# Kernel optimization log

Hardware: AMD Instinct MI355X
Metric: run time of the kernel (lower is better)

## Reference

```python
import jax, jax.numpy as jnp
import numpy as np


def _base_grid(B, H, W):
    xs = jnp.arange(W, dtype=jnp.float32)
    ys = jnp.arange(H, dtype=jnp.float32)
    gx, gy = jnp.meshgrid(xs, ys)  # [H,W] each, x varies along W
    return jnp.broadcast_to(jnp.stack([gx, gy], -1)[None], (B, H, W, 2))


def flow_to_grid(flow, accel=None):
    B, _, H, W = flow.shape
    v = 0.5 * flow
    if accel is not None:
        v = v + 0.25 * accel
    vgrid = _base_grid(B, H, W) + jnp.transpose(v, (0, 2, 3, 1))
    gx = 2.0 * vgrid[..., 0] / max(W - 1, 1) - 1.0
    gy = 2.0 * vgrid[..., 1] / max(H - 1, 1) - 1.0
    return jnp.stack([gx, gy], -1)  # [B,H,W,2]


def grid_sample_border(img, grid):
    # img [B,C,H,W], grid [B,Hg,Wg,2] normalized; bilinear, border pad, align_corners=True
    B, C, H, W = img.shape
    Hg, Wg = grid.shape[1], grid.shape[2]
    x = jnp.clip((grid[..., 0] + 1.0) * 0.5 * (W - 1), 0.0, W - 1)
    y = jnp.clip((grid[..., 1] + 1.0) * 0.5 * (H - 1), 0.0, H - 1)
    x0 = jnp.floor(x); y0 = jnp.floor(y)
    x1 = jnp.minimum(x0 + 1.0, W - 1); y1 = jnp.minimum(y0 + 1.0, H - 1)
    wx = (x - x0)[:, None]; wy = (y - y0)[:, None]  # [B,1,Hg,Wg]
    x0i, x1i, y0i, y1i = (a.astype(jnp.int32) for a in (x0, x1, y0, y1))
    flat = img.reshape(B, C, H * W)

    def gat(yi, xi):
        idx = jnp.broadcast_to((yi * W + xi).reshape(B, 1, Hg * Wg), (B, C, Hg * Wg))
        return jnp.take_along_axis(flat, idx, axis=2).reshape(B, C, Hg, Wg)

    v00, v01, v10, v11 = gat(y0i, x0i), gat(y0i, x1i), gat(y1i, x0i), gat(y1i, x1i)
    return v00 * (1 - wx) * (1 - wy) + v01 * wx * (1 - wy) + v10 * (1 - wx) * wy + v11 * wx * wy


def backward_warp(img, flow, accel=None):
    grid = flow_to_grid(flow, accel)
    warped = grid_sample_border(img, grid)
    valid = (jnp.abs(grid[..., 0]) <= 1.0) & (jnp.abs(grid[..., 1]) <= 1.0)
    return warped * valid[:, None].astype(img.dtype)


def local_kernel_warp(img, flow, kernel_params):
    B, C, H, W = img.shape
    k_row = jax.nn.softmax(kernel_params[:, :5], axis=1)   # [B,5,H,W]
    k_col = jax.nn.softmax(kernel_params[:, 5:10], axis=1)
    aniso = jax.nn.sigmoid(kernel_params[:, 10]) + 0.5     # [B,H,W]
    grid = flow_to_grid(flow)                               # [B,H,W,2]
    offsets = jnp.linspace(-2.0, 2.0, 5)
    a3 = aniso[..., None]                                   # [B,H,W,1]
    off_col = offsets.reshape(1, 1, 1, 5) * a3              # [B,H,W,5]
    off_row = offsets.reshape(1, 1, 1, 5) / a3
    zeros = jnp.zeros_like(off_row)
    grid_row = grid[:, :, :, None, :] + jnp.stack([off_row, zeros], -1) * (2.0 / W)
    samples_row = grid_sample_border(img, grid_row.reshape(B, H, W * 5, 2)).reshape(B, C, H, W, 5)
    img_row = jnp.einsum('bchwk,bkhw->bchw', samples_row, k_row)
    grid_base = flow_to_grid(jnp.zeros_like(flow))
    grid_col = grid_base[:, :, :, None, :] + jnp.stack([zeros, off_col], -1) * (2.0 / H)
    samples_col = grid_sample_border(img_row, grid_col.reshape(B, H, W * 5, 2)).reshape(B, C, H, W, 5)
    return jnp.einsum('bchwk,bkhw->bchw', samples_col, k_col)


def conv3x3(x, w, b):
    y = jax.lax.conv_general_dilated(x, w, (1, 1), 'SAME',
                                     dimension_numbers=('NCHW', 'OIHW', 'NCHW'))
    return y + b[None, :, None, None]


def reference(img, features, flow, kernel_params, w1, b1, w2, b2):
    B, _, H, W = img.shape
    Hf, Wf = features.shape[2], features.shape[3]
    warped_img = local_kernel_warp(img, flow, kernel_params)
    flow_scaled = jax.image.resize(flow, (B, 2, Hf, Wf), 'linear') * (Hf / H)
    warped_feat = backward_warp(features, flow_scaled)
    warped_img_down = jax.image.resize(warped_img, (B, 3, Hf, Wf), 'linear')
    x = jnp.concatenate([warped_feat, warped_img_down], axis=1)
    fused = conv3x3(jax.nn.relu(conv3x3(x, w1, b1)), w2, b2)
    return (warped_feat + fused, warped_img)


def setup_inputs() -> dict:
    key = jax.random.key(0)
    ks = jax.random.split(key, 6)
    B, H, W, Hf, Wf, Cf = 4, 512, 512, 256, 256, 96
    return {
        'img': jax.random.uniform(ks[0], (B, 3, H, W), jnp.float32),
        'features': jax.random.normal(ks[1], (B, Cf, Hf, Wf), jnp.float32),
        'flow': jax.random.normal(ks[2], (B, 2, H, W), jnp.float32) * 4.0,
        'kernel_params': jax.random.normal(ks[3], (B, 11, H, W), jnp.float32),
        'w1': jax.random.normal(ks[4], (Cf, Cf + 3, 3, 3), jnp.float32) * 0.02,
        'b1': jnp.zeros((Cf,), jnp.float32),
        'w2': jax.random.normal(ks[5], (Cf, Cf, 3, 3), jnp.float32) * 0.02,
        'b2': jnp.zeros((Cf,), jnp.float32),
    }
```

## Files before the change

kernel.cpp:

```cpp
#include <hip/hip_runtime.h>

#define NB 4
#define IH 512
#define IW 512
#define FH 256
#define FW 256
#define CF 96
#define C1 99
#define HWI (IH*IW)
#define HWF (FH*FW)
#define LDK 40

typedef short s8v __attribute__((ext_vector_type(8)));
typedef short s4v __attribute__((ext_vector_type(4)));
typedef float f4v __attribute__((ext_vector_type(4)));
typedef float f2v __attribute__((ext_vector_type(2), aligned(4)));

static __device__ __forceinline__ float sigmoidf_(float x) {
    return 1.0f / (1.0f + __expf(-x));
}
static __device__ __forceinline__ unsigned short f2bf(float f) {
    unsigned int u = __float_as_uint(f);
    unsigned int r = (u + 0x7fffu + ((u >> 16) & 1u)) >> 16;
    return (unsigned short)r;
}

__global__ __launch_bounds__(256)
void lkw_row_kernel(const float* __restrict__ img,
                    const float* __restrict__ flow,
                    const float* __restrict__ kp,
                    float* __restrict__ img_row) {
    int idx = blockIdx.x * blockDim.x + threadIdx.x;
    if (idx >= NB * HWI) return;
    int w = idx & (IW - 1);
    int h = (idx >> 9) & (IH - 1);
    int b = idx >> 18;

    const float* kpb = kp + (size_t)b * 11 * HWI + h * IW + w;
    float p[5];
    float m = -1e30f;
    #pragma unroll
    for (int k = 0; k < 5; k++) { p[k] = kpb[k * HWI]; m = fmaxf(m, p[k]); }
    float s = 0.f;
    #pragma unroll
    for (int k = 0; k < 5; k++) { p[k] = __expf(p[k] - m); s += p[k]; }
    float invs = 1.f / s;
    float a = sigmoidf_(kpb[10 * HWI]) + 0.5f;
    float inva = 1.f / a;

    float fx = flow[((size_t)b * 2 + 0) * HWI + h * IW + w];
    float fy = flow[((size_t)b * 2 + 1) * HWI + h * IW + w];

    float y = (float)h + 0.5f * fy;
    y = fminf(fmaxf(y, 0.f), (float)(IH - 1));
    float y0f = floorf(y);
    int y0 = (int)y0f;
    int y1 = min(y0 + 1, IH - 1);
    float wy = y - y0f;

    float xbase = (float)w + 0.5f * fx;
    const float sc = (float)(IW - 1) / (float)IW;

    const float* imb = img + (size_t)b * 3 * HWI;
    float acc0 = 0.f, acc1 = 0.f, acc2 = 0.f;
    #pragma unroll
    for (int k = 0; k < 5; k++) {
        float x = xbase + (float)(k - 2) * inva * sc;
        x = fminf(fmaxf(x, 0.f), (float)(IW - 1));
        float x0f = floorf(x);
        int x0 = (int)x0f;
        int x1 = min(x0 + 1, IW - 1);
        float wx = x - x0f;
        float wk = p[k] * invs;
        float w00 = (1.f - wx) * (1.f - wy) * wk;
        float w01 = wx * (1.f - wy) * wk;
        float w10 = (1.f - wx) * wy * wk;
        float w11 = wx * wy * wk;
        int i00 = y0 * IW + x0, i01 = y0 * IW + x1;
        int i10 = y1 * IW + x0, i11 = y1 * IW + x1;
        acc0 += w00 * imb[i00] + w01 * imb[i01] + w10 * imb[i10] + w11 * imb[i11];
        acc1 += w00 * imb[HWI + i00] + w01 * imb[HWI + i01] + w10 * imb[HWI + i10] + w11 * imb[HWI + i11];
        acc2 += w00 * imb[2 * HWI + i00] + w01 * imb[2 * HWI + i01] + w10 * imb[2 * HWI + i10] + w11 * imb[2 * HWI + i11];
    }
    img_row[(size_t)b * 3 * HWI + h * IW + w] = acc0;
    img_row[(size_t)b * 3 * HWI + HWI + h * IW + w] = acc1;
    img_row[(size_t)b * 3 * HWI + 2 * HWI + h * IW + w] = acc2;
}

__global__ __launch_bounds__(256)
void lkw_col_kernel(const float* __restrict__ img_row,
                    const float* __restrict__ kp,
                    float* __restrict__ out1) {
    int idx = blockIdx.x * blockDim.x + threadIdx.x;
    if (idx >= NB * HWI) return;
    int w = idx & (IW - 1);
    int h = (idx >> 9) & (IH - 1);
    int b = idx >> 18;

    const float* kpb = kp + (size_t)b * 11 * HWI + h * IW + w;
    float p[5];
    float m = -1e30f;
    #pragma unroll
    for (int k = 0; k < 5; k++) { p[k] = kpb[(5 + k) * HWI]; m = fmaxf(m, p[k]); }
    float s = 0.f;
    #pragma unroll
    for (int k = 0; k < 5; k++) { p[k] = __expf(p[k] - m); s += p[k]; }
    float invs = 1.f / s;
    float a = sigmoidf_(kpb[10 * HWI]) + 0.5f;

    const float sc = (float)(IH - 1) / (float)IH;
    const float* irb = img_row + (size_t)b * 3 * HWI;
    float acc0 = 0.f, acc1 = 0.f, acc2 = 0.f;
    #pragma unroll
    for (int k = 0; k < 5; k++) {
        float y = (float)h + (float)(k - 2) * a * sc;
        y = fminf(fmaxf(y, 0.f), (float)(IH - 1));
        float y0f = floorf(y);
        int y0 = (int)y0f;
        int y1 = min(y0 + 1, IH - 1);
        float wy = y - y0f;
        float wk = p[k] * invs;
        float w0 = (1.f - wy) * wk, w1 = wy * wk;
        int i0 = y0 * IW + w, i1 = y1 * IW + w;
        acc0 += w0 * irb[i0] + w1 * irb[i1];
        acc1 += w0 * irb[HWI + i0] + w1 * irb[HWI + i1];
        acc2 += w0 * irb[2 * HWI + i0] + w1 * irb[2 * HWI + i1];
    }
    out1[(size_t)b * 3 * HWI + h * IW + w] = acc0;
    out1[(size_t)b * 3 * HWI + HWI + h * IW + w] = acc1;
    out1[(size_t)b * 3 * HWI + 2 * HWI + h * IW + w] = acc2;
}

static __device__ __forceinline__ void ds_taps(int i, int n_in, int t[4], float wt[4]) {
    int n_out = n_in >> 1;
    if (i == 0) {
        t[0] = 0; t[1] = 0; t[2] = 1; t[3] = 2;
        wt[0] = 0.f; wt[1] = 3.f / 7.f; wt[2] = 3.f / 7.f; wt[3] = 1.f / 7.f;
    } else if (i == n_out - 1) {
        t[0] = n_in - 3; t[1] = n_in - 2; t[2] = n_in - 1; t[3] = n_in - 1;
        wt[0] = 1.f / 7.f; wt[1] = 3.f / 7.f; wt[2] = 3.f / 7.f; wt[3] = 0.f;
    } else {
        t[0] = 2 * i - 1; t[1] = 2 * i; t[2] = 2 * i + 1; t[3] = 2 * i + 2;
        wt[0] = 0.125f; wt[1] = 0.375f; wt[2] = 0.375f; wt[3] = 0.125f;
    }
}

__global__ __launch_bounds__(256)
void downsample2x_kernel(const float* __restrict__ src, float* __restrict__ dst,
                         int BC, float mul) {
    int idx = blockIdx.x * blockDim.x + threadIdx.x;
    if (idx >= BC * HWF) return;
    int j = idx & (FW - 1);
    int i = (idx >> 8) & (FH - 1);
    int bc = idx >> 16;

    int tx[4], ty[4];
    float wx[4], wy[4];
    ds_taps(j, IW, tx, wx);
    ds_taps(i, IH, ty, wy);
    const float* s = src + (size_t)bc * HWI;
    float acc = 0.f;
    #pragma unroll
    for (int a = 0; a < 4; a++) {
        if (wy[a] == 0.f) continue;
        const float* rp = s + (size_t)ty[a] * IW;
        float row = wx[0] * rp[tx[0]] + wx[1] * rp[tx[1]] + wx[2] * rp[tx[2]] + wx[3] * rp[tx[3]];
        acc += wy[a] * row;
    }
    dst[idx] = acc * mul;
}

__global__ __launch_bounds__(256)
void imgdown_cl_kernel(const float* __restrict__ out1, short* __restrict__ xin) {
    int idx = blockIdx.x * blockDim.x + threadIdx.x;
    if (idx >= NB * HWF) return;
    int j = idx & (FW - 1);
    int i = (idx >> 8) & (FH - 1);
    int b = idx >> 16;

    int tx[4], ty[4];
    float wx[4], wy[4];
    ds_taps(j, IW, tx, wx);
    ds_taps(i, IH, ty, wy);
    const float* s = out1 + (size_t)b * 3 * HWI;
    float acc[3] = {0.f, 0.f, 0.f};
    #pragma unroll
    for (int a = 0; a < 4; a++) {
        if (wy[a] == 0.f) continue;
        #pragma unroll
        for (int c = 0; c < 3; c++) {
            const float* rp = s + (size_t)c * HWI + (size_t)ty[a] * IW;
            float row = wx[0] * rp[tx[0]] + wx[1] * rp[tx[1]] + wx[2] * rp[tx[2]] + wx[3] * rp[tx[3]];
            acc[c] += wy[a] * row;
        }
    }
    short* dst = xin + ((size_t)(b * FH + i) * FW + j) * 128 + 96;
    s8v g0 = { (short)f2bf(acc[0]), (short)f2bf(acc[1]), (short)f2bf(acc[2]), 0, 0, 0, 0, 0 };
    s8v z  = { 0, 0, 0, 0, 0, 0, 0, 0 };
    *(s8v*)(dst)      = g0;
    *(s8v*)(dst + 8)  = z;
    *(s8v*)(dst + 16) = z;
    *(s8v*)(dst + 24) = z;
}

__global__ __launch_bounds__(256)
void warp_feat_cl_kernel(const float* __restrict__ feat,
                         const float* __restrict__ flow_s,
                         float* __restrict__ wfeat,
                         short* __restrict__ xin) {
    int t = blockIdx.x * 256 + threadIdx.x;
    int g = t & 7;
    int pix = t >> 3;
    int j = pix & (FW - 1);
    int i = (pix >> 8) & (FH - 1);
    int b = pix >> 16;

    float fx = flow_s[((size_t)b * 2 + 0) * HWF + i * FW + j];
    float fy = flow_s[((size_t)b * 2 + 1) * HWF + i * FW + j];
    float u = (float)j + 0.5f * fx;
    float v = (float)i + 0.5f * fy;
    bool valid = (u >= 0.f) && (u <= (float)(FW - 1)) && (v >= 0.f) && (v <= (float)(FH - 1));
    float x = fminf(fmaxf(u, 0.f), (float)(FW - 1));
    float y = fminf(fmaxf(v, 0.f), (float)(FH - 1));
    int x0 = min((int)x, FW - 2);
    int y0 = min((int)y, FH - 2);
    float wxf = x - (float)x0, wyf = y - (float)y0;
    float w00 = (1.f - wxf) * (1.f - wyf), w01 = wxf * (1.f - wyf);
    float w10 = (1.f - wxf) * wyf, w11 = wxf * wyf;
    if (!valid) { w00 = w01 = w10 = w11 = 0.f; }

    const float* fb = feat + ((size_t)b * CF + g * 12) * HWF + (size_t)y0 * FW + x0;
    float vals[12];
    #pragma unroll
    for (int k = 0; k < 12; k++) {
        const float* p = fb + (size_t)k * HWF;
        f2v r0 = *(const f2v*)p;
        f2v r1 = *(const f2v*)(p + FW);
        vals[k] = w00 * r0.x + w01 * r0.y + w10 * r1.x + w11 * r1.y;
    }

    float* ob = wfeat + ((size_t)b * CF + g * 12) * HWF + (size_t)i * FW + j;
    #pragma unroll
    for (int k = 0; k < 12; k++) ob[(size_t)k * HWF] = vals[k];

    short* xr = xin + (size_t)pix * 128 + g * 12;
    #pragma unroll
    for (int q2 = 0; q2 < 3; q2++) {
        s4v pk = { (short)f2bf(vals[q2 * 4 + 0]), (short)f2bf(vals[q2 * 4 + 1]),
                   (short)f2bf(vals[q2 * 4 + 2]), (short)f2bf(vals[q2 * 4 + 3]) };
        *(s4v*)(xr + q2 * 4) = pk;
    }
}

__global__ __launch_bounds__(256)
void cvt_w1_kernel(const float* __restrict__ w1, short* __restrict__ wA1) {
    int i = blockIdx.x * 256 + threadIdx.x;
    if (i >= 9 * 96 * 128) return;
    int ci = i & 127;
    int co = (i >> 7) % 96;
    int off = i / (96 * 128);
    float v = (ci < C1) ? w1[((size_t)co * C1 + ci) * 9 + off] : 0.f;
    wA1[i] = (short)f2bf(v);
}
__global__ __launch_bounds__(256)
void cvt_w2_kernel(const float* __restrict__ w2, short* __restrict__ wA2) {
    int i = blockIdx.x * 256 + threadIdx.x;
    if (i >= 9 * 96 * 96) return;
    int ci = i % 96;
    int co = (i / 96) % 96;
    int off = i / (96 * 96);
    wA2[i] = (short)f2bf(w2[((size_t)co * CF + ci) * 9 + off]);
}

template <int PASS>
__global__ __launch_bounds__(256)
void conv_mfma_kernel(const short* __restrict__ X,
                      const short* __restrict__ W,
                      const float* __restrict__ bias,
                      short* __restrict__ t1out,
                      float* __restrict__ out0) {
    constexpr int KSTR = (PASS == 1) ? 128 : 96;
    constexpr int KC = KSTR / 32;
    __shared__ short Als[96 * LDK];
    __shared__ short Bls[128 * LDK];

    const int bx = blockIdx.x;
    const int w0 = (bx & 1) * 128;
    const int h  = (bx >> 1) & (FH - 1);
    const int b  = bx >> 9;

    const int tid = threadIdx.x;
    const int lane = tid & 63;
    const int wv = tid >> 6;
    const int ln = lane & 15;
    const int q  = lane >> 4;

    f4v acc[6][2];
    #pragma unroll
    for (int mt = 0; mt < 6; mt++)
        #pragma unroll
        for (int nt = 0; nt < 2; nt++)
            acc[mt][nt] = (f4v){0.f, 0.f, 0.f, 0.f};

    const short* Xb = X + (size_t)(b * FH) * FW * KSTR;

    const int an = tid >> 1, ah = tid & 1;

    for (int off = 0; off < 9; ++off) {
        const int dy = off / 3 - 1, dx = off % 3 - 1;
        const int hy = h + dy;
        const bool hok = (hy >= 0) && (hy < FH);
        const short* Xrow = Xb + (size_t)hy * FW * KSTR;
        const short* Woff = W + (size_t)off * 96 * KSTR;
        const int wc = w0 + an + dx;
        const bool cok = hok && (wc >= 0) && (wc < FW);

        for (int kc = 0; kc < KC; ++kc) {
            const int ci0 = kc * 32;
            __syncthreads();
            if (tid < 192) {
                const short* srcA = Woff + (size_t)an * KSTR + ci0 + ah * 16;
                short* dstA = Als + an * LDK + ah * 16;
                *(float4*)dstA = *(const float4*)srcA;
                *(float4*)(dstA + 8) = *(const float4*)(srcA + 8);
            }
            {
                float4 vb0 = {0.f, 0.f, 0.f, 0.f};
                float4 vb1 = {0.f, 0.f, 0.f, 0.f};
                if (cok) {
                    const short* srcB = Xrow + (size_t)wc * KSTR + ci0 + ah * 16;
                    vb0 = *(const float4*)srcB;
                    vb1 = *(const float4*)(srcB + 8);
                }
                short* dstB = Bls + an * LDK + ah * 16;
                *(float4*)dstB = vb0;
                *(float4*)(dstB + 8) = vb1;
            }
            __syncthreads();
            s8v bfr0 = *(const s8v*)(Bls + (wv * 32 + ln) * LDK + q * 8);
            s8v bfr1 = *(const s8v*)(Bls + (wv * 32 + 16 + ln) * LDK + q * 8);
            #pragma unroll
            for (int mt = 0; mt < 6; ++mt) {
                s8v afr = *(const s8v*)(Als + (mt * 16 + ln) * LDK + q * 8);
                acc[mt][0] = __builtin_amdgcn_mfma_f32_16x16x32_bf16(afr, bfr0, acc[mt][0], 0, 0, 0);
                acc[mt][1] = __builtin_amdgcn_mfma_f32_16x16x32_bf16(afr, bfr1, acc[mt][1], 0, 0, 0);
            }
        }
    }

    if (PASS == 1) {
        const size_t rowbase = (size_t)(b * FH + h) * FW;
        #pragma unroll
        for (int nt = 0; nt < 2; ++nt) {
            int pos = w0 + wv * 32 + nt * 16 + ln;
            short* dst = t1out + (rowbase + pos) * CF;
            #pragma unroll
            for (int mt = 0; mt < 6; ++mt) {
                int co0 = mt * 16 + q * 4;
                s4v pk;
                #pragma unroll
                for (int r = 0; r < 4; ++r) {
                    float v = acc[mt][nt][r] + bias[co0 + r];
                    pk[r] = (short)f2bf(fmaxf(v, 0.f));
                }
                *(s4v*)(dst + co0) = pk;
            }
        }
    } else {
        #pragma unroll
        for (int nt = 0; nt < 2; ++nt) {
            int pos = w0 + wv * 32 + nt * 16 + ln;
            #pragma unroll
            for (int mt = 0; mt < 6; ++mt) {
                int co0 = mt * 16 + q * 4;
                #pragma unroll
                for (int r = 0; r < 4; ++r) {
                    size_t o = (size_t)(b * CF + co0 + r) * HWF + (size_t)h * FW + pos;
                    out0[o] += acc[mt][nt][r] + bias[co0 + r];
                }
            }
        }
    }
}

extern "C" void kernel_launch(void* const* d_in, const int* in_sizes, int n_in,
                              void* d_out, int out_size, void* d_ws, size_t ws_size,
                              hipStream_t stream) {
    const float* img  = (const float*)d_in[0];
    const float* feat = (const float*)d_in[1];
    const float* flow = (const float*)d_in[2];
    const float* kp   = (const float*)d_in[3];
    const float* w1   = (const float*)d_in[4];
    const float* b1   = (const float*)d_in[5];
    const float* w2   = (const float*)d_in[6];
    const float* b2   = (const float*)d_in[7];

    float* out0 = (float*)d_out;
    float* out1 = out0 + (size_t)NB * CF * HWF;

    char* wsb = (char*)d_ws;
    short* wA1 = (short*)wsb;
    short* wA2 = (short*)(wsb + 221184);
    short* xin = (short*)(wsb + 221184 + 165888);
    char* region = wsb + 221184 + 165888 + 67108864;
    short* t1cl    = (short*)region;
    float* img_row = (float*)region;
    float* flow_s  = (float*)(region + 16777216);

    int n_img = NB * HWI;
    hipLaunchKernelGGL(cvt_w1_kernel, dim3((9 * 96 * 128 + 255) / 256), dim3(256), 0, stream, w1, wA1);
    hipLaunchKernelGGL(cvt_w2_kernel, dim3((9 * 96 * 96 + 255) / 256), dim3(256), 0, stream, w2, wA2);
    hipLaunchKernelGGL(lkw_row_kernel, dim3((n_img + 255) / 256), dim3(256), 0, stream,
                       img, flow, kp, img_row);
    hipLaunchKernelGGL(lkw_col_kernel, dim3((n_img + 255) / 256), dim3(256), 0, stream,
                       img_row, kp, out1);
    hipLaunchKernelGGL(downsample2x_kernel, dim3((NB * 2 * HWF + 255) / 256), dim3(256), 0, stream,
                       flow, flow_s, NB * 2, 0.5f);
    hipLaunchKernelGGL(imgdown_cl_kernel, dim3((NB * HWF + 255) / 256), dim3(256), 0, stream,
                       out1, xin);
    hipLaunchKernelGGL(warp_feat_cl_kernel, dim3(NB * HWF * 8 / 256), dim3(256), 0, stream,
                       feat, flow_s, out0, xin);
    hipLaunchKernelGGL((conv_mfma_kernel<1>), dim3(NB * FH * 2), dim3(256), 0, stream,
                       xin, wA1, b1, t1cl, (float*)nullptr);
    hipLaunchKernelGGL((conv_mfma_kernel<2>), dim3(NB * FH * 2), dim3(256), 0, stream,
                       t1cl, wA2, b2, (short*)nullptr, out0);
}
```

Baseline: 687.8 us.

## Transpose features to channels-last before warping for coalesced bilinear gathers

Adds a shared-memory transpose kernel that rewrites the NCHW feature map into a channels-last buffer, in fp32 when the workspace is large enough and bf16 otherwise. A new warp kernel then gathers the four bilinear corners as contiguous channel vectors instead of strided per-channel reads. This targets the scattered gather traffic in the feature warp. The cost is an extra full pass over the features and a larger workspace, with the old path kept as a fallback when the workspace is too small.

```diff
diff --git a/kernel.cpp b/kernel.cpp
--- a/kernel.cpp
+++ b/kernel.cpp
@@ -23,6 +23,10 @@
     unsigned int u = __float_as_uint(f);
     unsigned int r = (u + 0x7fffu + ((u >> 16) & 1u)) >> 16;
     return (unsigned short)r;
+}
+static __device__ __forceinline__ float bf2f(short s) {
+    unsigned int u = ((unsigned int)(unsigned short)s) << 16;
+    return __uint_as_float(u);
 }
 
 __global__ __launch_bounds__(256)
@@ -201,6 +205,115 @@
     *(s8v*)(dst + 8)  = z;
     *(s8v*)(dst + 16) = z;
     *(s8v*)(dst + 24) = z;
+}
+
+template <int BF>
+__global__ __launch_bounds__(256)
+void feat_cl_kernel(const float* __restrict__ feat, void* __restrict__ featT) {
+    __shared__ float tile[64 * 97];
+    int blk = blockIdx.x;
+    int b = blk >> 10;
+    int p0 = (blk & 1023) << 6;
+    int t = threadIdx.x;
+    {
+        int px = t & 63, cq = t >> 6;
+        const float* src = feat + (size_t)b * CF * HWF + p0 + px;
+        #pragma unroll
+        for (int k = 0; k < 24; k++) {
+            int c = cq * 24 + k;
+            tile[px * 97 + c] = src[(size_t)c * HWF];
+        }
+    }
+    __syncthreads();
+    int pxo = t >> 2, co = (t & 3) * 24;
+    const float* trow = &tile[pxo * 97 + co];
+    size_t obase = ((size_t)(b * HWF) + p0 + pxo) * 96 + co;
+    if (BF) {
+        short* dst = (short*)featT + obase;
+        #pragma unroll
+        for (int q = 0; q < 3; q++) {
+            s8v pk;
+            #pragma unroll
+            for (int e = 0; e < 8; e++) pk[e] = (short)f2bf(trow[q * 8 + e]);
+            *(s8v*)(dst + q * 8) = pk;
+        }
+    } else {
+        float* dst = (float*)featT + obase;
+        #pragma unroll
+        for (int q = 0; q < 6; q++) {
+            f4v vv = { trow[q * 4 + 0], trow[q * 4 + 1], trow[q * 4 + 2], trow[q * 4 + 3] };
+            *(f4v*)(dst + q * 4) = vv;
+        }
+    }
+}
+
+template <int BF>
+__global__ __launch_bounds__(256)
+void warp_feat_cl2_kernel(const void* __restrict__ featT,
+                          const float* __restrict__ flow_s,
+                          float* __restrict__ wfeat,
+                          short* __restrict__ xin) {
+    int t = blockIdx.x * 256 + threadIdx.x;
+    int g = t & 7;
+    int pix = t >> 3;
+    int j = pix & (FW - 1);
+    int i = (pix >> 8) & (FH - 1);
+    int b = pix >> 16;
+
+    float fx = flow_s[((size_t)b * 2 + 0) * HWF + i * FW + j];
+    float fy = flow_s[((size_t)b * 2 + 1) * HWF + i * FW + j];
+    float u = (float)j + 0.5f * fx;
+    float v = (float)i + 0.5f * fy;
+    bool valid = (u >= 0.f) && (u <= (float)(FW - 1)) && (v >= 0.f) && (v <= (float)(FH - 1));
+    float x = fminf(fmaxf(u, 0.f), (float)(FW - 1));
+    float y = fminf(fmaxf(v, 0.f), (float)(FH - 1));
+    int x0 = min((int)x, FW - 2);
+    int y0 = min((int)y, FH - 2);
+    float wxf = x - (float)x0, wyf = y - (float)y0;
+    float w00 = (1.f - wxf) * (1.f - wyf), w01 = wxf * (1.f - wyf);
+    float w10 = (1.f - wxf) * wyf, w11 = wxf * wyf;
+    if (!valid) { w00 = w01 = w10 = w11 = 0.f; }
+
+    size_t base = ((size_t)(b * HWF) + (size_t)y0 * FW + x0) * 96 + g * 12;
+    float vals[12];
+    if (BF) {
+        const short* fp = (const short*)featT + base;
+        #pragma unroll
+        for (int q = 0; q < 3; q++) {
+            s4v a0 = *(const s4v*)(fp + q * 4);
+            s4v a1 = *(const s4v*)(fp + 96 + q * 4);
+            s4v a2 = *(const s4v*)(fp + 96 * FW + q * 4);
+            s4v a3 = *(const s4v*)(fp + 96 * FW + 96 + q * 4);
+            #pragma unroll
+            for (int e = 0; e < 4; e++)
+                vals[q * 4 + e] = w00 * bf2f(a0[e]) + w01 * bf2f(a1[e])
+                                + w10 * bf2f(a2[e]) + w11 * bf2f(a3[e]);
+        }
+    } else {
+        const float* fp = (const float*)featT + base;
+        #pragma unroll
+        for (int q = 0; q < 3; q++) {
+            f4v a0 = *(const f4v*)(fp + q * 4);
+            f4v a1 = *(const f4v*)(fp + 96 + q * 4);
+            f4v a2 = *(const f4v*)(fp + 96 * FW + q * 4);
+            f4v a3 = *(const f4v*)(fp + 96 * FW + 96 + q * 4);
+            #pragma unroll
+            for (int e = 0; e < 4; e++)
+                vals[q * 4 + e] = w00 * a0[e] + w01 * a1[e] + w10 * a2[e] + w11 * a3[e];
+        }
+    }
+
+    float* ob = wfeat + ((size_t)b * CF + g * 12) * HWF + (size_t)i * FW + j;
+    #pragma unroll
+    for (int k = 0; k < 12; k++) ob[(size_t)k * HWF] = vals[k];
+
+    short* xr = xin + (size_t)pix * 128 + g * 12;
+    #pragma unroll
+    for (int q2 = 0; q2 < 3; q2++) {
+        s4v pk = { (short)f2bf(vals[q2 * 4 + 0]), (short)f2bf(vals[q2 * 4 + 1]),
+                   (short)f2bf(vals[q2 * 4 + 2]), (short)f2bf(vals[q2 * 4 + 3]) };
+        *(s4v*)(xr + q2 * 4) = pk;
+    }
 }
 
 __global__ __launch_bounds__(256)
@@ -401,27 +514,69 @@
     char* wsb = (char*)d_ws;
     short* wA1 = (short*)wsb;
     short* wA2 = (short*)(wsb + 221184);
-    short* xin = (short*)(wsb + 221184 + 165888);
-    char* region = wsb + 221184 + 165888 + 67108864;
-    short* t1cl    = (short*)region;
-    float* img_row = (float*)region;
-    float* flow_s  = (float*)(region + 16777216);
+    short* xin = (short*)(wsb + 387072);
+    const size_t off_after_xin = 387072 + 67108864;
+
+    const size_t FEATT_F32 = (size_t)NB * HWF * 96 * 4;
+    const size_t FEATT_BF16 = (size_t)NB * HWF * 96 * 2;
+    const size_t FLOW_B = 2097152;
+    const size_t need_f32 = off_after_xin + FLOW_B + FEATT_F32;
+    const size_t need_b16 = off_after_xin + FLOW_B + FEATT_BF16;
 
     int n_img = NB * HWI;
     hipLaunchKernelGGL(cvt_w1_kernel, dim3((9 * 96 * 128 + 255) / 256), dim3(256), 0, stream, w1, wA1);
     hipLaunchKernelGGL(cvt_w2_kernel, dim3((9 * 96 * 96 + 255) / 256), dim3(256), 0, stream, w2, wA2);
-    hipLaunchKernelGGL(lkw_row_kernel, dim3((n_img + 255) / 256), dim3(256), 0, stream,
-                       img, flow, kp, img_row);
-    hipLaunchKernelGGL(lkw_col_kernel, dim3((n_img + 255) / 256), dim3(256), 0, stream,
-                       img_row, kp, out1);
-    hipLaunchKernelGGL(downsample2x_kernel, dim3((NB * 2 * HWF + 255) / 256), dim3(256), 0, stream,
-                       flow, flow_s, NB * 2, 0.5f);
-    hipLaunchKernelGGL(imgdown_cl_kernel, dim3((NB * HWF + 255) / 256), dim3(256), 0, stream,
-                       out1, xin);
-    hipLaunchKernelGGL(warp_feat_cl_kernel, dim3(NB * HWF * 8 / 256), dim3(256), 0, stream,
-                       feat, flow_s, out0, xin);
-    hipLaunchKernelGGL((conv_mfma_kernel<1>), dim3(NB * FH * 2), dim3(256), 0, stream,
-                       xin, wA1, b1, t1cl, (float*)nullptr);
-    hipLaunchKernelGGL((conv_mfma_kernel<2>), dim3(NB * FH * 2), dim3(256), 0, stream,
-                       t1cl, wA2, b2, (short*)nullptr, out0);
-}
+
+    if (ws_size >= need_b16) {
+        const bool f32ok = (ws_size >= need_f32);
+        float* flow_s = (float*)(wsb + off_after_xin);
+        char* region  = wsb + off_after_xin + FLOW_B;
+        float* img_row = (float*)region;
+        void*  featT   = (void*)region;
+        short* t1cl    = (short*)region;
+
+        hipLaunchKernelGGL(lkw_row_kernel, dim3((n_img + 255) / 256), dim3(256), 0, stream,
+                           img, flow, kp, img_row);
+        hipLaunchKernelGGL(lkw_col_kernel, dim3((n_img + 255) / 256), dim3(256), 0, stream,
+                           img_row, kp, out1);
+        hipLaunchKernelGGL(downsample2x_kernel, dim3((NB * 2 * HWF + 255) / 256), dim3(256), 0, stream,
+                           flow, flow_s, NB * 2, 0.5f);
+        hipLaunchKernelGGL(imgdown_cl_kernel, dim3((NB * HWF + 255) / 256), dim3(256), 0, stream,
+                           out1, xin);
+        if (f32ok) {
+            hipLaunchKernelGGL((feat_cl_kernel<0>), dim3(NB * (HWF / 64)), dim3(256), 0, stream,
+                               feat, featT);
+            hipLaunchKernelGGL((warp_feat_cl2_kernel<0>), dim3(NB * HWF * 8 / 256), dim3(256), 0, stream,
+                               featT, flow_s, out0, xin);
+        } else {
+            hipLaunchKernelGGL((feat_cl_kernel<1>), dim3(NB * (HWF / 64)), dim3(256), 0, stream,
+                               feat, featT);
+            hipLaunchKernelGGL((warp_feat_cl2_kernel<1>), dim3(NB * HWF * 8 / 256), dim3(256), 0, stream,
+                               featT, flow_s, out0, xin);
+        }
+        hipLaunchKernelGGL((conv_mfma_kernel<1>), dim3(NB * FH * 2), dim3(256), 0, stream,
+                           xin, wA1, b1, t1cl, (float*)nullptr);
+        hipLaunchKernelGGL((conv_mfma_kernel<2>), dim3(NB * FH * 2), dim3(256), 0, stream,
+                           t1cl, wA2, b2, (short*)nullptr, out0);
+    } else {
+        char* region = wsb + off_after_xin;
+        short* t1cl    = (short*)region;
+        float* img_row = (float*)region;
+        float* flow_s  = (float*)(region + 16777216);
+
+        hipLaunchKernelGGL(lkw_row_kernel, dim3((n_img + 255) / 256), dim3(256), 0, stream,
+                           img, flow, kp, img_row);
+        hipLaunchKernelGGL(lkw_col_kernel, dim3((n_img + 255) / 256), dim3(256), 0, stream,
+                           img_row, kp, out1);
+        hipLaunchKernelGGL(downsample2x_kernel, dim3((NB * 2 * HWF + 255) / 256), dim3(256), 0, stream,
+                           flow, flow_s, NB * 2, 0.5f);
+        hipLaunchKernelGGL(imgdown_cl_kernel, dim3((NB * HWF + 255) / 256), dim3(256), 0, stream,
+                           out1, xin);
+        hipLaunchKernelGGL(warp_feat_cl_kernel, dim3(NB * HWF * 8 / 256), dim3(256), 0, stream,
+                           feat, flow_s, out0, xin);
+        hipLaunchKernelGGL((conv_mfma_kernel<1>), dim3(NB * FH * 2), dim3(256), 0, stream,
+                           xin, wA1, b1, t1cl, (float*)nullptr);
+        hipLaunchKernelGGL((conv_mfma_kernel<2>), dim3(NB * FH * 2), dim3(256), 0, stream,
+                           t1cl, wA2, b2, (short*)nullptr, out0);
+    }
+}
```

Result: faster. 664.0 us (-3.5%).
